# Kernel tuning notes

Measured on AMD Instinct MI355X. Metric: run time of the kernel, lower is better.

## Reference

```python
import jax, jax.numpy as jnp
import numpy as np

B, C, K = 8, 32, 512


def setup_inputs() -> dict:
    key = jax.random.key(0)
    k1, k2, k3 = jax.random.split(key, 3)
    amplitude = jax.random.normal(k1, (B, C, K), dtype=jnp.float32)
    phase = jax.random.normal(k2, (B, C, K), dtype=jnp.float32)
    A = jax.random.normal(k3, (K, K), dtype=jnp.float32)
    w_amplitude = jnp.float32(0.5)
    w_phase = jnp.float32(0.5)
    return {"amplitude": amplitude, "phase": phase, "A": A,
            "w_amplitude": w_amplitude, "w_phase": w_phase}


def reference(amplitude, phase, A, w_amplitude, w_phase):
    # amplitude, phase: (B, C, K)
    # pairwise differences along the frequency axis -> (B, C, K, K)
    amp_diff = amplitude[..., :, None] - amplitude[..., None, :]
    ph_diff = phase[..., :, None] - phase[..., None, :]
    fused = w_amplitude * amp_diff + w_phase * ph_diff
    # einsum('dd,bxcd->bxcd', A, fused): scale last axis by diag(A)
    temp = fused * jnp.diagonal(A)
    # einsum('bxcd,bxcd->bcd'): sum of squares over channel axis x=C -> (B, K, K)
    dist = jnp.sum(temp * temp, axis=1)
    exp_dist = 1.0 / (dist + 1e-10)
    eye = jnp.eye(K, dtype=exp_dist.dtype)
    offdiag = 1.0 - eye
    exp_dist = exp_dist * offdiag
    exp_max = jax.lax.stop_gradient(jnp.max(exp_dist, axis=-1, keepdims=True))
    p = exp_dist / exp_max
    p = (p * offdiag + eye) * 0.99  # probabilities in (0, 0.99]
    # bernoulli gumbel-softmax (hard, tau=1) with straight-through estimator
    logit = jnp.log(p / (1.0 - p))          # log(p/(1-p)); other class is -logit
    logits = jnp.stack([logit, -logit], axis=-1)  # (B, K, K, 2)
    gkey = jax.random.key(42)
    u = jax.random.uniform(gkey, logits.shape, minval=1e-10, maxval=1.0)
    gumbel = -jnp.log(-jnp.log(u))
    y_soft = jax.nn.softmax(logits + gumbel, axis=-1)
    idx = jnp.argmax(y_soft, axis=-1)
    y_hard = jax.nn.one_hot(idx, 2, dtype=y_soft.dtype)
    y = y_hard + y_soft - jax.lax.stop_gradient(y_soft)
    sample = y[..., 0]  # (B, K, K)
    return sample.mean(axis=0)  # (K, K)
```

## Files before the change

kernel.cpp:

```cpp
#include <hip/hip_runtime.h>
#include <stdint.h>
#include <math.h>

constexpr int NB = 8;
constexpr int NC = 32;
constexpr int NK = 512;
constexpr int ROWS = 4;

__device__ __forceinline__ uint32_t rotl32(uint32_t x, uint32_t r) {
    return (x << r) | (x >> (32u - r));
}

__device__ __forceinline__ uint32_t jax_random_bits(uint32_t n) {
    const uint32_t k0 = 0u, k1 = 42u;
    const uint32_t ks2 = k0 ^ k1 ^ 0x1BD11BDAu;
    uint32_t x0 = 0u + k0, x1 = n + k1;

    x0 += x1; x1 = rotl32(x1, 13); x1 ^= x0;
    x0 += x1; x1 = rotl32(x1, 15); x1 ^= x0;
    x0 += x1; x1 = rotl32(x1, 26); x1 ^= x0;
    x0 += x1; x1 = rotl32(x1,  6); x1 ^= x0;
    x0 += k1; x1 += ks2 + 1u;

    x0 += x1; x1 = rotl32(x1, 17); x1 ^= x0;
    x0 += x1; x1 = rotl32(x1, 29); x1 ^= x0;
    x0 += x1; x1 = rotl32(x1, 16); x1 ^= x0;
    x0 += x1; x1 = rotl32(x1, 24); x1 ^= x0;
    x0 += ks2; x1 += k0 + 2u;

    x0 += x1; x1 = rotl32(x1, 13); x1 ^= x0;
    x0 += x1; x1 = rotl32(x1, 15); x1 ^= x0;
    x0 += x1; x1 = rotl32(x1, 26); x1 ^= x0;
    x0 += x1; x1 = rotl32(x1,  6); x1 ^= x0;
    x0 += k0; x1 += k1 + 3u;

    x0 += x1; x1 = rotl32(x1, 17); x1 ^= x0;
    x0 += x1; x1 = rotl32(x1, 29); x1 ^= x0;
    x0 += x1; x1 = rotl32(x1, 16); x1 ^= x0;
    x0 += x1; x1 = rotl32(x1, 24); x1 ^= x0;
    x0 += k1; x1 += ks2 + 4u;

    x0 += x1; x1 = rotl32(x1, 13); x1 ^= x0;
    x0 += x1; x1 = rotl32(x1, 15); x1 ^= x0;
    x0 += x1; x1 = rotl32(x1, 26); x1 ^= x0;
    x0 += x1; x1 = rotl32(x1,  6); x1 ^= x0;
    x0 += ks2; x1 += k0 + 5u;

    return x0 ^ x1;
}

__device__ __forceinline__ float fastL(uint32_t bits, double& ud) {
    const double S = 1.0 - 1e-10, T = 1e-10;
    uint32_t fb = (bits >> 9) | 0x3F800000u;
    float bf = __uint_as_float(fb) - 1.0f;
    ud = (double)bf * S + T;
    if (bf <= 0.5f) {
        return -logf((float)ud);
    } else {
        double vm1 = S * ((double)bf - 1.0);
        return -log1pf((float)vm1);
    }
}

__device__ __forceinline__ bool decide(double D, double q ,
                                       bool diag, uint32_t n0) {
    uint32_t bits0 = jax_random_bits(n0);
    uint32_t bits1 = jax_random_bits(n0 + 1u);
    double u0d, u1d;
    float L0f = fastL(bits0, u0d);
    float L1f = fastL(bits1, u1d);

    double a2d, c2d;
    if (diag) { a2d = 9801.0; c2d = 1.0; }
    else      { a2d = q * q; double t = D - q; c2d = t * t; }

    float lhs = (float)a2d * L1f;
    float rhs = (float)c2d * L0f;
    float diff = lhs - rhs;
    if (fabsf(diff) > 1e-4f * (lhs + rhs))
        return diff >= 0.0f;

    double L0 = -log(u0d);
    double L1 = -log(u1d);
    return a2d * L1 >= c2d * L0;
}

__global__ void prep_kernel(const float* __restrict__ amp,
                            const float* __restrict__ ph,
                            const float* __restrict__ A,
                            const float* __restrict__ wav,
                            const float* __restrict__ wpv,
                            double* __restrict__ F,
                            double* __restrict__ Ad2,
                            float* __restrict__ out) {
    int t = blockIdx.x * 256 + threadIdx.x;
    out[t] = 0.0f;
    if (t < NB * NC * NK) {
        double wa = (double)wav[0], wp = (double)wpv[0];
        F[t] = wa * (double)amp[t] + wp * (double)ph[t];
    }
    if (t < NK) {
        double a = (double)A[t * NK + t];
        Ad2[t] = a * a;
    }
}

__global__ __launch_bounds__(256) void sample_kernel(
    const double* __restrict__ F, const double* __restrict__ Ad2,
    float* __restrict__ out)
{
    const int i0  = blockIdx.x * ROWS;
    const int b   = blockIdx.y;
    const int tid = threadIdx.x;

    __shared__ double fi[ROWS][NC];
    __shared__ double sred[ROWS][4];
    __shared__ double s_q[ROWS];

    const double* Fb = F + (size_t)b * NC * NK;

    if (tid < ROWS * NC) {
        int r = tid >> 5, c = tid & 31;
        fi[r][c] = Fb[c * NK + (i0 + r)];
    }
    __syncthreads();

    double acc[2][ROWS];
    #pragma unroll
    for (int it = 0; it < 2; ++it)
        #pragma unroll
        for (int r = 0; r < ROWS; ++r) acc[it][r] = 0.0;

    #pragma unroll 4
    for (int c = 0; c < NC; ++c) {
        double fj0 = Fb[c * NK + tid];
        double fj1 = Fb[c * NK + tid + 256];
        #pragma unroll
        for (int r = 0; r < ROWS; ++r) {
            double fic = fi[r][c];
            double d0 = fic - fj0; acc[0][r] = fma(d0, d0, acc[0][r]);
            double d1 = fic - fj1; acc[1][r] = fma(d1, d1, acc[1][r]);
        }
    }

    double D[2][ROWS];
    #pragma unroll
    for (int it = 0; it < 2; ++it) {
        int j = tid + it * 256;
        double a2 = Ad2[j];
        #pragma unroll
        for (int r = 0; r < ROWS; ++r) {
            double dist = acc[it][r] * a2;
            D[it][r] = dist + 1e-10;
        }
    }

    #pragma unroll
    for (int r = 0; r < ROWS; ++r) {
        const int i = i0 + r;
        double m = 1e300;
        #pragma unroll
        for (int it = 0; it < 2; ++it) {
            int j = tid + it * 256;
            if (j != i) m = fmin(m, D[it][r]);
        }
        #pragma unroll
        for (int off = 32; off > 0; off >>= 1)
            m = fmin(m, __shfl_down(m, off));
        if ((tid & 63) == 0) sred[r][tid >> 6] = m;
    }
    __syncthreads();
    if (tid < ROWS) {
        double m = fmin(fmin(sred[tid][0], sred[tid][1]),
                        fmin(sred[tid][2], sred[tid][3]));
        s_q[tid] = 0.99 * m;
    }
    __syncthreads();

    #pragma unroll
    for (int it = 0; it < 2; ++it) {
        const int j = tid + it * 256;
        #pragma unroll
        for (int r = 0; r < ROWS; ++r) {
            const int i = i0 + r;
            uint32_t n0 = 2u * (((uint32_t)(b * NK + i)) * NK + (uint32_t)j);
            if (decide(D[it][r], s_q[r], j == i, n0))
                atomicAdd(&out[i * NK + j], 0.125f);
        }
    }
}

extern "C" void kernel_launch(void* const* d_in, const int* in_sizes, int n_in,
                              void* d_out, int out_size, void* d_ws, size_t ws_size,
                              hipStream_t stream) {
    const float* amp = (const float*)d_in[0];
    const float* ph  = (const float*)d_in[1];
    const float* A   = (const float*)d_in[2];
    const float* wa  = (const float*)d_in[3];
    const float* wp  = (const float*)d_in[4];
    float* out = (float*)d_out;

    double* F   = (double*)d_ws;
    double* Ad2 = (double*)d_ws + NB * NC * NK;

    prep_kernel<<<1024, 256, 0, stream>>>(amp, ph, A, wa, wp, F, Ad2, out);

    dim3 grid(NK / ROWS, NB);
    sample_kernel<<<grid, 256, 0, stream>>>(F, Ad2, out);
}
```

Baseline: 93.60 us.

## Fuse prep into sampler, early-reject tiny probabilities, outline slow log path

Drops the prep kernel that materialised the weighted double-precision F array and Ad2. The sampler now reads amp/phase as floats (float2 per thread, contiguous j pair) and computes the weighted values and the diagonal of A inline. The output zeroing moves to a small float4 kernel. decide() now returns false before generating Threefry bits when c2 is far larger than a2, which skips RNG and log work for most off-diagonal entries. The double-precision log fallback is moved into a noinline function to reduce register pressure. The trade-offs are recomputing F per block and a rejection threshold that must be conservative enough to never change a sample.

```diff
diff --git a/kernel.cpp b/kernel.cpp
--- a/kernel.cpp
+++ b/kernel.cpp
@@ -62,68 +62,57 @@
     }
 }
 
+__device__ __noinline__ bool decide_slow(double a2, double c2,
+                                         double u0, double u1) {
+    return a2 * (-log(u1)) >= c2 * (-log(u0));
+}
+
 __device__ __forceinline__ bool decide(double D, double q ,
                                        bool diag, uint32_t n0) {
+    double a2, c2;
+    if (diag) { a2 = 9801.0; c2 = 1.0; }
+    else {
+        a2 = q * q;
+        double t = D - q;
+        c2 = t * t;
+        if (c2 > 1.95e8 * a2) return false;
+    }
     uint32_t bits0 = jax_random_bits(n0);
     uint32_t bits1 = jax_random_bits(n0 + 1u);
     double u0d, u1d;
     float L0f = fastL(bits0, u0d);
     float L1f = fastL(bits1, u1d);
 
-    double a2d, c2d;
-    if (diag) { a2d = 9801.0; c2d = 1.0; }
-    else      { a2d = q * q; double t = D - q; c2d = t * t; }
-
-    float lhs = (float)a2d * L1f;
-    float rhs = (float)c2d * L0f;
+    float lhs = (float)a2 * L1f;
+    float rhs = (float)c2 * L0f;
     float diff = lhs - rhs;
     if (fabsf(diff) > 1e-4f * (lhs + rhs))
         return diff >= 0.0f;
-
-    double L0 = -log(u0d);
-    double L1 = -log(u1d);
-    return a2d * L1 >= c2d * L0;
-}
-
-__global__ void prep_kernel(const float* __restrict__ amp,
-                            const float* __restrict__ ph,
-                            const float* __restrict__ A,
-                            const float* __restrict__ wav,
-                            const float* __restrict__ wpv,
-                            double* __restrict__ F,
-                            double* __restrict__ Ad2,
-                            float* __restrict__ out) {
-    int t = blockIdx.x * 256 + threadIdx.x;
-    out[t] = 0.0f;
-    if (t < NB * NC * NK) {
-        double wa = (double)wav[0], wp = (double)wpv[0];
-        F[t] = wa * (double)amp[t] + wp * (double)ph[t];
-    }
-    if (t < NK) {
-        double a = (double)A[t * NK + t];
-        Ad2[t] = a * a;
-    }
+    return decide_slow(a2, c2, u0d, u1d);
+}
+
+__global__ void zero_out_kernel(float4* __restrict__ out) {
+    out[blockIdx.x * blockDim.x + threadIdx.x] = make_float4(0.f, 0.f, 0.f, 0.f);
 }
 
 __global__ __launch_bounds__(256) void sample_kernel(
-    const double* __restrict__ F, const double* __restrict__ Ad2,
-    float* __restrict__ out)
+    const float* __restrict__ amp, const float* __restrict__ ph,
+    const float* __restrict__ A, const float* __restrict__ wav,
+    const float* __restrict__ wpv, float* __restrict__ out)
 {
     const int i0  = blockIdx.x * ROWS;
     const int b   = blockIdx.y;
     const int tid = threadIdx.x;
-
-    __shared__ double fi[ROWS][NC];
+    const int j0  = 2 * tid;
+
     __shared__ double sred[ROWS][4];
     __shared__ double s_q[ROWS];
 
-    const double* Fb = F + (size_t)b * NC * NK;
-
-    if (tid < ROWS * NC) {
-        int r = tid >> 5, c = tid & 31;
-        fi[r][c] = Fb[c * NK + (i0 + r)];
-    }
-    __syncthreads();
+    const double wa = (double)wav[0];
+    const double wp = (double)wpv[0];
+
+    const float* __restrict__ ab = amp + (size_t)b * NC * NK;
+    const float* __restrict__ pb = ph  + (size_t)b * NC * NK;
 
     double acc[2][ROWS];
     #pragma unroll
@@ -133,26 +122,33 @@
 
     #pragma unroll 4
     for (int c = 0; c < NC; ++c) {
-        double fj0 = Fb[c * NK + tid];
-        double fj1 = Fb[c * NK + tid + 256];
+        double fi_r[ROWS];
         #pragma unroll
         for (int r = 0; r < ROWS; ++r) {
-            double fic = fi[r][c];
-            double d0 = fic - fj0; acc[0][r] = fma(d0, d0, acc[0][r]);
-            double d1 = fic - fj1; acc[1][r] = fma(d1, d1, acc[1][r]);
+            float ai = ab[c * NK + i0 + r];
+            float pi = pb[c * NK + i0 + r];
+            fi_r[r] = wa * (double)ai + wp * (double)pi;
+        }
+        float2 av = *(const float2*)(ab + c * NK + j0);
+        float2 pv = *(const float2*)(pb + c * NK + j0);
+        double fj0 = wa * (double)av.x + wp * (double)pv.x;
+        double fj1 = wa * (double)av.y + wp * (double)pv.y;
+        #pragma unroll
+        for (int r = 0; r < ROWS; ++r) {
+            double d0 = fi_r[r] - fj0; acc[0][r] = fma(d0, d0, acc[0][r]);
+            double d1 = fi_r[r] - fj1; acc[1][r] = fma(d1, d1, acc[1][r]);
         }
     }
 
     double D[2][ROWS];
     #pragma unroll
     for (int it = 0; it < 2; ++it) {
-        int j = tid + it * 256;
-        double a2 = Ad2[j];
-        #pragma unroll
-        for (int r = 0; r < ROWS; ++r) {
-            double dist = acc[it][r] * a2;
-            D[it][r] = dist + 1e-10;
-        }
+        int j = j0 + it;
+        double ad = (double)A[j * NK + j];
+        double a2 = ad * ad;
+        #pragma unroll
+        for (int r = 0; r < ROWS; ++r)
+            D[it][r] = acc[it][r] * a2 + 1e-10;
     }
 
     #pragma unroll
@@ -161,7 +157,7 @@
         double m = 1e300;
         #pragma unroll
         for (int it = 0; it < 2; ++it) {
-            int j = tid + it * 256;
+            int j = j0 + it;
             if (j != i) m = fmin(m, D[it][r]);
         }
         #pragma unroll
@@ -179,7 +175,7 @@
 
     #pragma unroll
     for (int it = 0; it < 2; ++it) {
-        const int j = tid + it * 256;
+        const int j = j0 + it;
         #pragma unroll
         for (int r = 0; r < ROWS; ++r) {
             const int i = i0 + r;
@@ -200,11 +196,8 @@
     const float* wp  = (const float*)d_in[4];
     float* out = (float*)d_out;
 
-    double* F   = (double*)d_ws;
-    double* Ad2 = (double*)d_ws + NB * NC * NK;
-
-    prep_kernel<<<1024, 256, 0, stream>>>(amp, ph, A, wa, wp, F, Ad2, out);
+    zero_out_kernel<<<256, 256, 0, stream>>>((float4*)out);
 
     dim3 grid(NK / ROWS, NB);
-    sample_kernel<<<grid, 256, 0, stream>>>(F, Ad2, out);
-}
+    sample_kernel<<<grid, 256, 0, stream>>>(amp, ph, A, wa, wp, out);
+}
```

Result: slower. 100.7 us (+7.6%).

## Skip RNG for pairs whose outcome is fixed and compact remaining work per wave

Applied to the files above, without the earlier changes.

Adds a per-pair bound test. It uses the fact that the ratio of the two -log(u) terms cannot exceed about 1.95e8 given the uniform's float granularity and 1e-10 floor. Pairs whose (D-q)^2 exceeds that multiple of q^2 are known to sample zero, so their Threefry hashes and logs are skipped. Pairs that still need sampling are compacted per wave with ballot and popcount into shared-memory lists, so the costly RNG work runs on dense lanes. Rows per block drop from 4 to 2, each thread now handles two adjacent columns with double2 loads, and the rare double-precision fallback is moved into a noinline function to cut register pressure. The risk is correctness if the bound is not conservative, plus extra overhead from shuffles and shared-memory traffic.

```diff
diff --git a/kernel.cpp b/kernel.cpp
--- a/kernel.cpp
+++ b/kernel.cpp
@@ -5,7 +5,7 @@
 constexpr int NB = 8;
 constexpr int NC = 32;
 constexpr int NK = 512;
-constexpr int ROWS = 4;
+constexpr int ROWS = 2;
 
 __device__ __forceinline__ uint32_t rotl32(uint32_t x, uint32_t r) {
     return (x << r) | (x >> (32u - r));
@@ -62,27 +62,29 @@
     }
 }
 
-__device__ __forceinline__ bool decide(double D, double q ,
-                                       bool diag, uint32_t n0) {
+__device__ __noinline__ bool decide_slow(double a2, double c2,
+                                         double u0, double u1) {
+    return a2 * (-log(u1)) >= c2 * (-log(u0));
+}
+
+__device__ __forceinline__ bool decide_rng(double D, double q ,
+                                           bool diag, uint32_t n0) {
+    double a2, c2;
+    if (diag) { a2 = 9801.0; c2 = 1.0; }
+    else      { a2 = q * q; double t = D - q; c2 = t * t; }
+
     uint32_t bits0 = jax_random_bits(n0);
     uint32_t bits1 = jax_random_bits(n0 + 1u);
     double u0d, u1d;
     float L0f = fastL(bits0, u0d);
     float L1f = fastL(bits1, u1d);
 
-    double a2d, c2d;
-    if (diag) { a2d = 9801.0; c2d = 1.0; }
-    else      { a2d = q * q; double t = D - q; c2d = t * t; }
-
-    float lhs = (float)a2d * L1f;
-    float rhs = (float)c2d * L0f;
+    float lhs = (float)a2 * L1f;
+    float rhs = (float)c2 * L0f;
     float diff = lhs - rhs;
     if (fabsf(diff) > 1e-4f * (lhs + rhs))
         return diff >= 0.0f;
-
-    double L0 = -log(u0d);
-    double L1 = -log(u1d);
-    return a2d * L1 >= c2d * L0;
+    return decide_slow(a2, c2, u0d, u1d);
 }
 
 __global__ void prep_kernel(const float* __restrict__ amp,
@@ -91,7 +93,7 @@
                             const float* __restrict__ wav,
                             const float* __restrict__ wpv,
                             double* __restrict__ F,
-                            double* __restrict__ Ad2,
+                            double* __restrict__ A2,
                             float* __restrict__ out) {
     int t = blockIdx.x * 256 + threadIdx.x;
     out[t] = 0.0f;
@@ -101,29 +103,27 @@
     }
     if (t < NK) {
         double a = (double)A[t * NK + t];
-        Ad2[t] = a * a;
+        A2[t] = a * a;
     }
 }
 
 __global__ __launch_bounds__(256) void sample_kernel(
-    const double* __restrict__ F, const double* __restrict__ Ad2,
+    const double* __restrict__ F, const double* __restrict__ A2,
     float* __restrict__ out)
 {
-    const int i0  = blockIdx.x * ROWS;
-    const int b   = blockIdx.y;
-    const int tid = threadIdx.x;
-
-    __shared__ double fi[ROWS][NC];
+    const int i0   = blockIdx.x * ROWS;
+    const int b    = blockIdx.y;
+    const int tid  = threadIdx.x;
+    const int j0   = 2 * tid;
+    const int lane = tid & 63;
+    const int wv   = tid >> 6;
+    const int wjb  = wv * 128;
+
+    __shared__ unsigned char wlist[4][ROWS][128];
     __shared__ double sred[ROWS][4];
     __shared__ double s_q[ROWS];
 
-    const double* Fb = F + (size_t)b * NC * NK;
-
-    if (tid < ROWS * NC) {
-        int r = tid >> 5, c = tid & 31;
-        fi[r][c] = Fb[c * NK + (i0 + r)];
-    }
-    __syncthreads();
+    const double* __restrict__ Fb = F + (size_t)b * NC * NK;
 
     double acc[2][ROWS];
     #pragma unroll
@@ -133,41 +133,33 @@
 
     #pragma unroll 4
     for (int c = 0; c < NC; ++c) {
-        double fj0 = Fb[c * NK + tid];
-        double fj1 = Fb[c * NK + tid + 256];
-        #pragma unroll
-        for (int r = 0; r < ROWS; ++r) {
-            double fic = fi[r][c];
-            double d0 = fic - fj0; acc[0][r] = fma(d0, d0, acc[0][r]);
-            double d1 = fic - fj1; acc[1][r] = fma(d1, d1, acc[1][r]);
-        }
-    }
-
+        double fr0 = Fb[c * NK + i0];
+        double fr1 = Fb[c * NK + i0 + 1];
+        double2 fj = *(const double2*)(Fb + c * NK + j0);
+        double d00 = fr0 - fj.x; acc[0][0] = fma(d00, d00, acc[0][0]);
+        double d10 = fr0 - fj.y; acc[1][0] = fma(d10, d10, acc[1][0]);
+        double d01 = fr1 - fj.x; acc[0][1] = fma(d01, d01, acc[0][1]);
+        double d11 = fr1 - fj.y; acc[1][1] = fma(d11, d11, acc[1][1]);
+    }
+
+    double2 a2j = *(const double2*)(A2 + j0);
     double D[2][ROWS];
     #pragma unroll
-    for (int it = 0; it < 2; ++it) {
-        int j = tid + it * 256;
-        double a2 = Ad2[j];
-        #pragma unroll
-        for (int r = 0; r < ROWS; ++r) {
-            double dist = acc[it][r] * a2;
-            D[it][r] = dist + 1e-10;
-        }
+    for (int r = 0; r < ROWS; ++r) {
+        D[0][r] = acc[0][r] * a2j.x + 1e-10;
+        D[1][r] = acc[1][r] * a2j.y + 1e-10;
     }
 
     #pragma unroll
     for (int r = 0; r < ROWS; ++r) {
         const int i = i0 + r;
         double m = 1e300;
-        #pragma unroll
-        for (int it = 0; it < 2; ++it) {
-            int j = tid + it * 256;
-            if (j != i) m = fmin(m, D[it][r]);
-        }
+        if (j0     != i) m = fmin(m, D[0][r]);
+        if (j0 + 1 != i) m = fmin(m, D[1][r]);
         #pragma unroll
         for (int off = 32; off > 0; off >>= 1)
             m = fmin(m, __shfl_down(m, off));
-        if ((tid & 63) == 0) sred[r][tid >> 6] = m;
+        if (lane == 0) sred[r][wv] = m;
     }
     __syncthreads();
     if (tid < ROWS) {
@@ -177,14 +169,41 @@
     }
     __syncthreads();
 
-    #pragma unroll
-    for (int it = 0; it < 2; ++it) {
-        const int j = tid + it * 256;
-        #pragma unroll
-        for (int r = 0; r < ROWS; ++r) {
-            const int i = i0 + r;
+    const unsigned long long ltmask = (1ull << lane) - 1ull;
+    int nw[ROWS];
+    #pragma unroll
+    for (int r = 0; r < ROWS; ++r) {
+        const int i = i0 + r;
+        const double q = s_q[r];
+        const double thr = 1.95e8 * (q * q);
+        double t0 = D[0][r] - q;
+        double t1 = D[1][r] - q;
+        bool need0 = (j0     == i) || !(t0 * t0 > thr);
+        bool need1 = (j0 + 1 == i) || !(t1 * t1 > thr);
+        unsigned long long m0 = __ballot(need0);
+        unsigned long long m1 = __ballot(need1);
+        int c0 = __popcll(m0);
+        nw[r] = c0 + __popcll(m1);
+        if (need0) wlist[wv][r][__popcll(m0 & ltmask)]      = (unsigned char)(2 * lane);
+        if (need1) wlist[wv][r][c0 + __popcll(m1 & ltmask)] = (unsigned char)(2 * lane + 1);
+    }
+
+    #pragma unroll
+    for (int r = 0; r < ROWS; ++r) {
+        const int i = i0 + r;
+        const double q = s_q[r];
+        const int n = nw[r];
+        for (int k0v = 0; k0v < n; k0v += 64) {
+            int k = k0v + lane;
+            bool act = k < n;
+            int jl = wlist[wv][r][act ? k : 0];
+            int src = jl >> 1;
+            double d0s = __shfl(D[0][r], src);
+            double d1s = __shfl(D[1][r], src);
+            double Dv = (jl & 1) ? d1s : d0s;
+            int j = wjb + jl;
             uint32_t n0 = 2u * (((uint32_t)(b * NK + i)) * NK + (uint32_t)j);
-            if (decide(D[it][r], s_q[r], j == i, n0))
+            if (act && decide_rng(Dv, q, j == i, n0))
                 atomicAdd(&out[i * NK + j], 0.125f);
         }
     }
@@ -200,11 +219,11 @@
     const float* wp  = (const float*)d_in[4];
     float* out = (float*)d_out;
 
-    double* F   = (double*)d_ws;
-    double* Ad2 = (double*)d_ws + NB * NC * NK;
-
-    prep_kernel<<<1024, 256, 0, stream>>>(amp, ph, A, wa, wp, F, Ad2, out);
+    double* F  = (double*)d_ws;
+    double* A2 = (double*)d_ws + NB * NC * NK;
+
+    prep_kernel<<<1024, 256, 0, stream>>>(amp, ph, A, wa, wp, F, A2, out);
 
     dim3 grid(NK / ROWS, NB);
-    sample_kernel<<<grid, 256, 0, stream>>>(F, Ad2, out);
-}
+    sample_kernel<<<grid, 256, 0, stream>>>(F, A2, out);
+}
```

New measurement: 84.92 us. 9.3% less time.
